# Performance work log

Measured on AMD Instinct MI355X. Metric: run time of the kernel, lower is better.

## Reference

```python
import jax, jax.numpy as jnp
import numpy as np

D_MODEL = 768
D_COND = 128
N_LAYERS = 6
D_STATE = 16
D_CONV = 4
EXPAND = 2
D_INNER = EXPAND * D_MODEL            # 1536
DT_RANK = (D_MODEL + 15) // 16        # 48
BATCH, SEQ = 2, 1024
EPS = 1e-5


def setup_inputs() -> dict:
    key = jax.random.key(0)
    ks = iter(jax.random.split(key, 24))
    rn = lambda shape, s=0.02: jax.random.normal(next(ks), shape, dtype=jnp.float32) * s
    inp = {}
    inp["x"] = jax.random.normal(next(ks), (BATCH, SEQ, D_MODEL), dtype=jnp.float32)
    inp["condition"] = jax.random.normal(next(ks), (BATCH, D_COND), dtype=jnp.float32)
    # per-layer Mamba params, stacked on leading layer dim
    inp["in_proj_w"] = rn((N_LAYERS, 2 * D_INNER, D_MODEL))
    inp["conv_w"] = rn((N_LAYERS, D_INNER, D_CONV), 0.1)
    inp["conv_b"] = jnp.zeros((N_LAYERS, D_INNER), jnp.float32)
    inp["x_proj_w"] = rn((N_LAYERS, DT_RANK + 2 * D_STATE, D_INNER))
    inp["dt_proj_w"] = rn((N_LAYERS, D_INNER, DT_RANK), 0.1)
    inp["dt_proj_b"] = jnp.full((N_LAYERS, D_INNER), -4.0, jnp.float32)  # softplus -> small dt
    inp["A_log"] = jnp.tile(jnp.log(jnp.arange(1, D_STATE + 1, dtype=jnp.float32))[None, None, :], (N_LAYERS, D_INNER, 1))
    inp["D_skip"] = jnp.ones((N_LAYERS, D_INNER), jnp.float32)
    inp["out_proj_w"] = rn((N_LAYERS, D_MODEL, D_INNER))
    # post-residual LayerNorm affine per layer
    inp["norm_w"] = jnp.ones((N_LAYERS, D_MODEL), jnp.float32)
    inp["norm_b"] = jnp.zeros((N_LAYERS, D_MODEL), jnp.float32)
    # AdaLN: condition -> (scale, shift)
    inp["adaln_w"] = rn((N_LAYERS, 2 * D_MODEL, D_COND))
    inp["adaln_b"] = jnp.zeros((N_LAYERS, 2 * D_MODEL), jnp.float32)
    inp["final_norm_w"] = jnp.ones((D_MODEL,), jnp.float32)
    inp["final_norm_b"] = jnp.zeros((D_MODEL,), jnp.float32)
    return inp


def _ln(h, w, b):
    mu = jnp.mean(h, -1, keepdims=True)
    var = jnp.mean(jnp.square(h - mu), -1, keepdims=True)
    return (h - mu) * jax.lax.rsqrt(var + EPS) * w + b


def _ln_noaffine(h):
    mu = jnp.mean(h, -1, keepdims=True)
    var = jnp.mean(jnp.square(h - mu), -1, keepdims=True)
    return (h - mu) * jax.lax.rsqrt(var + EPS)


def _mamba(x, in_w, cw, cb, xp_w, dtp_w, dtp_b, A_log, D_skip, out_w):
    b, l, _ = x.shape
    xz = jnp.einsum('bld,ed->ble', x, in_w)                 # [b,l,2*di]
    xc, z = jnp.split(xz, 2, axis=-1)
    # causal depthwise conv over time
    xc_t = jnp.transpose(xc, (0, 2, 1))                     # [b,di,l]
    xc_t = jax.lax.conv_general_dilated(
        xc_t, cw[:, None, :], window_strides=(1,), padding=[(D_CONV - 1, 0)],
        dimension_numbers=('NCH', 'OIH', 'NCH'), feature_group_count=D_INNER)
    xc = jnp.transpose(xc_t + cb[None, :, None], (0, 2, 1))  # [b,l,di]
    xc = jax.nn.silu(xc)
    dbc = jnp.einsum('bld,ed->ble', xc, xp_w)                # [b,l,dt_rank+2*ds]
    dt = dbc[..., :DT_RANK]
    Bm = dbc[..., DT_RANK:DT_RANK + D_STATE]                 # [b,l,ds]
    Cm = dbc[..., DT_RANK + D_STATE:]                        # [b,l,ds]
    dt = jax.nn.softplus(jnp.einsum('blr,dr->bld', dt, dtp_w) + dtp_b)  # [b,l,di]
    A = -jnp.exp(A_log)                                      # [di,ds]

    def step(h, ts):
        dt_t, B_t, C_t, x_t = ts                             # [b,di],[b,ds],[b,ds],[b,di]
        dA = jnp.exp(dt_t[:, :, None] * A)                   # [b,di,ds]
        h = dA * h + (dt_t * x_t)[:, :, None] * B_t[:, None, :]
        y = jnp.sum(h * C_t[:, None, :], axis=-1)            # [b,di]
        return h, y

    h0 = jnp.zeros((b, D_INNER, D_STATE), x.dtype)
    ts = (jnp.transpose(dt, (1, 0, 2)), jnp.transpose(Bm, (1, 0, 2)),
          jnp.transpose(Cm, (1, 0, 2)), jnp.transpose(xc, (1, 0, 2)))
    h_final, y = jax.lax.scan(step, h0, ts)
    y = jnp.transpose(y, (1, 0, 2)) + D_skip * xc            # [b,l,di]
    y = y * jax.nn.silu(z)
    out = jnp.einsum('bld,ed->ble', y, out_w)                # [b,l,dm]
    return out, h_final


def reference(x, condition, in_proj_w, conv_w, conv_b, x_proj_w, dt_proj_w, dt_proj_b,
              A_log, D_skip, out_proj_w, norm_w, norm_b, adaln_w, adaln_b,
              final_norm_w, final_norm_b):
    h = x
    states = []
    for i in range(N_LAYERS):
        residual = h
        m, st = _mamba(h, in_proj_w[i], conv_w[i], conv_b[i], x_proj_w[i],
                       dt_proj_w[i], dt_proj_b[i], A_log[i], D_skip[i], out_proj_w[i])
        h = _ln(residual + m, norm_w[i], norm_b[i])
        ss = condition @ adaln_w[i].T + adaln_b[i]            # [b,2*dm]
        scale, shift = jnp.split(ss, 2, axis=-1)
        h = _ln_noaffine(h) * (1.0 + scale[:, None, :]) + shift[:, None, :]
        states.append(st)
    h = _ln(h, final_norm_w, final_norm_b)
    return h, jnp.stack(states)
```

## Files before the change

kernel.cpp:

```cpp
#include <hip/hip_runtime.h>
#include <hip/hip_bf16.h>

#define NL 6
#define DM 768
#define DI 1536
#define DS 16
#define NRANK 48
#define DBC 80
#define BATCH 2
#define SEQ 1024
#define NTOK (BATCH*SEQ)
#define NCHUNK 64
#define CHLEN 16
#define XKS 8
#define XKC (DI/XKS)

typedef __attribute__((ext_vector_type(8))) short short8;
typedef __attribute__((ext_vector_type(4))) float f32x4;
typedef __attribute__((ext_vector_type(4))) unsigned short ushort4v;

__device__ inline unsigned short f2bf(float f) {
  union { float f; unsigned u; } x; x.f = f;
  unsigned r = x.u + 0x7FFF + ((x.u >> 16) & 1);
  return (unsigned short)(r >> 16);
}
__device__ inline float bf2f(unsigned short s) {
  union { unsigned u; float f; } x; x.u = ((unsigned)s) << 16;
  return x.f;
}

__device__ inline void gl_lds16(const unsigned short* g, unsigned short* l) {
  __builtin_amdgcn_global_load_lds(
      (const __attribute__((address_space(1))) unsigned int*)(g),
      (__attribute__((address_space(3))) unsigned int*)(l),
      16, 0, 0);
}

#define SPAN_X   (NTOK * DM / 4)
#define SPAN_INW (NL * 2 * DI * DM / 4)
#define SPAN_OUW (NL * DM * DI / 4)
#define SPAN_XPW (NL * DBC * DI / 4)
#define SPAN_ALL (SPAN_X + SPAN_INW + SPAN_OUW + SPAN_XPW)

__device__ inline void cvt4_store(const float* s, unsigned short* d, int i) {
  f32x4 v = ((const f32x4*)s)[i];
  union { ushort4v u4; __hip_bfloat162 h[2]; } u;
  float2 p;
  p.x = v[0]; p.y = v[1]; u.h[0] = __float22bfloat162_rn(p);
  p.x = v[2]; p.y = v[3]; u.h[1] = __float22bfloat162_rn(p);
  ((ushort4v*)d)[i] = u.u4;
}

__global__ __launch_bounds__(256) void cvtall_k(const float* __restrict__ x,
                                                const float* __restrict__ inw,
                                                const float* __restrict__ ouw,
                                                const float* __restrict__ xpw,
                                                unsigned short* __restrict__ xb,
                                                unsigned short* __restrict__ inwb,
                                                unsigned short* __restrict__ ouwb,
                                                unsigned short* __restrict__ xpwb) {
  for (int i = blockIdx.x * 256 + threadIdx.x; i < SPAN_ALL; i += gridDim.x * 256) {
    if (i < SPAN_X) cvt4_store(x, xb, i);
    else if (i < SPAN_X + SPAN_INW) cvt4_store(inw, inwb, i - SPAN_X);
    else if (i < SPAN_X + SPAN_INW + SPAN_OUW) cvt4_store(ouw, ouwb, i - SPAN_X - SPAN_INW);
    else cvt4_store(xpw, xpwb, i - SPAN_X - SPAN_INW - SPAN_OUW);
  }
}

__global__ __launch_bounds__(256) void misc_pre_k(const float* __restrict__ w,
                                                  const float* __restrict__ al,
                                                  unsigned short* __restrict__ wb,
                                                  float* __restrict__ na) {
  int idx = blockIdx.x * 256 + threadIdx.x;
  const int NDT = NL * 1536 * 64;
  if (idx < NDT) {
    int col = idx & 63;
    int row = idx >> 6;
    wb[idx] = (col < NRANK) ? f2bf(w[(size_t)row * NRANK + col]) : (unsigned short)0;
  } else if (idx < NDT + NL * DI * DS) {
    int k = idx - NDT;
    na[k] = -__expf(al[k]);
  }
}

__global__ __launch_bounds__(256) void bt128b_k(
    const unsigned short* __restrict__ A, int lda,
    const unsigned short* __restrict__ W, int ldw,
    unsigned short* __restrict__ C, int ldc,
    int K) {
  __shared__ __align__(16) unsigned short As[2][128 * 32];
  __shared__ __align__(16) unsigned short Ws[2][128 * 32];
  const int tid = threadIdx.x;
  const int bm = blockIdx.y * 128;
  const int bn = blockIdx.x * 128;
  const int lane = tid & 63;
  const int wv = tid >> 6;
  const int wm = (wv >> 1) * 64;
  const int wn = (wv & 1) * 64;
  const int fr = lane & 15;
  const int fs = lane >> 4;

  const int r0 = tid >> 2;
  const int s0 = (tid & 3) ^ (r0 & 3);

  const unsigned short* gA0 = A + (size_t)(bm + r0) * lda + s0 * 8;
  const unsigned short* gA1 = A + (size_t)(bm + r0 + 64) * lda + s0 * 8;
  const unsigned short* gW0 = W + (size_t)(bn + r0) * ldw + s0 * 8;
  const unsigned short* gW1 = W + (size_t)(bn + r0 + 64) * ldw + s0 * 8;

  f32x4 acc[4][4];
#pragma unroll
  for (int i = 0; i < 4; i++)
#pragma unroll
    for (int j = 0; j < 4; j++) acc[i][j] = (f32x4){0.f, 0.f, 0.f, 0.f};

  gl_lds16(gA0, &As[0][0] + tid * 8);
  gl_lds16(gA1, &As[0][2048] + tid * 8);
  gl_lds16(gW0, &Ws[0][0] + tid * 8);
  gl_lds16(gW1, &Ws[0][2048] + tid * 8);
  __syncthreads();

  const int nk = K >> 5;
  int buf = 0;
  for (int kk = 0; kk < nk; kk++) {
    if (kk + 1 < nk) {
      const int k0 = (kk + 1) * 32;
      gl_lds16(gA0 + k0, &As[buf ^ 1][0] + tid * 8);
      gl_lds16(gA1 + k0, &As[buf ^ 1][2048] + tid * 8);
      gl_lds16(gW0 + k0, &Ws[buf ^ 1][0] + tid * 8);
      gl_lds16(gW1 + k0, &Ws[buf ^ 1][2048] + tid * 8);
    }

    short8 af[4], bf[4];
#pragma unroll
    for (int i = 0; i < 4; i++) {
      int rowa = wm + i * 16 + fr;
      af[i] = *(const short8*)&As[buf][rowa * 32 + ((fs ^ (rowa & 3)) * 8)];
      int rowb = wn + i * 16 + fr;
      bf[i] = *(const short8*)&Ws[buf][rowb * 32 + ((fs ^ (rowb & 3)) * 8)];
    }
#pragma unroll
    for (int i = 0; i < 4; i++)
#pragma unroll
      for (int j = 0; j < 4; j++)
        acc[i][j] = __builtin_amdgcn_mfma_f32_16x16x32_bf16(af[i], bf[j], acc[i][j], 0, 0, 0);

    __syncthreads();
    buf ^= 1;
  }

#pragma unroll
  for (int i = 0; i < 4; i++) {
#pragma unroll
    for (int j = 0; j < 4; j++) {
#pragma unroll
      for (int r = 0; r < 4; r++) {
        int row = bm + wm + i * 16 + fs * 4 + r;
        int col = bn + wn + j * 16 + fr;
        C[(size_t)row * ldc + col] = f2bf(acc[i][j][r]);
      }
    }
  }
}

template<int EPI>
__global__ __launch_bounds__(256) void bt64_k(
    const unsigned short* __restrict__ A, int lda,
    const unsigned short* __restrict__ W, int ldw,
    void* __restrict__ Cv, int ldc,
    int K,
    const float* __restrict__ bias,
    const float* __restrict__ resid) {
  __shared__ __align__(16) unsigned short As[2][64 * 32];
  __shared__ __align__(16) unsigned short Ws[2][64 * 32];
  const int tid = threadIdx.x;
  const int bm = blockIdx.y * 64;
  const int bn = blockIdx.x * 64;
  const int lane = tid & 63;
  const int wv = tid >> 6;
  const int wm = (wv >> 1) * 32;
  const int wn = (wv & 1) * 32;
  const int fr = lane & 15;
  const int fs = lane >> 4;

  const int r0 = tid >> 2;
  const int s0 = (tid & 3) ^ (r0 & 3);

  const unsigned short* gA = A + (size_t)(bm + r0) * lda + s0 * 8;
  const unsigned short* gW = W + (size_t)(bn + r0) * ldw + s0 * 8;

  f32x4 acc[2][2];
#pragma unroll
  for (int i = 0; i < 2; i++)
#pragma unroll
    for (int j = 0; j < 2; j++) acc[i][j] = (f32x4){0.f, 0.f, 0.f, 0.f};

  gl_lds16(gA, &As[0][0] + tid * 8);
  gl_lds16(gW, &Ws[0][0] + tid * 8);
  __syncthreads();

  const int nk = K >> 5;
  int buf = 0;
  for (int kk = 0; kk < nk; kk++) {
    if (kk + 1 < nk) {
      const int k0 = (kk + 1) * 32;
      gl_lds16(gA + k0, &As[buf ^ 1][0] + tid * 8);
      gl_lds16(gW + k0, &Ws[buf ^ 1][0] + tid * 8);
    }

    short8 af[2], bf[2];
#pragma unroll
    for (int i = 0; i < 2; i++) {
      int rowa = wm + i * 16 + fr;
      af[i] = *(const short8*)&As[buf][rowa * 32 + ((fs ^ (rowa & 3)) * 8)];
      int rowb = wn + i * 16 + fr;
      bf[i] = *(const short8*)&Ws[buf][rowb * 32 + ((fs ^ (rowb & 3)) * 8)];
    }
#pragma unroll
    for (int i = 0; i < 2; i++)
#pragma unroll
      for (int j = 0; j < 2; j++)
        acc[i][j] = __builtin_amdgcn_mfma_f32_16x16x32_bf16(af[i], bf[j], acc[i][j], 0, 0, 0);

    __syncthreads();
    buf ^= 1;
  }

#pragma unroll
  for (int i = 0; i < 2; i++) {
#pragma unroll
    for (int j = 0; j < 2; j++) {
#pragma unroll
      for (int r = 0; r < 4; r++) {
        int row = bm + wm + i * 16 + fs * 4 + r;
        int col = bn + wn + j * 16 + fr;
        float v = acc[i][j][r];
        if (EPI == 1) {
          float xv = v + bias[col];
          float sp = (xv > 20.f) ? xv : log1pf(__expf(xv));
          ((unsigned short*)Cv)[(size_t)row * ldc + col] = f2bf(sp);
        }
        if (EPI == 2) {
          ((float*)Cv)[(size_t)row * ldc + col] = v + resid[(size_t)row * ldc + col];
        }
      }
    }
  }
}

__global__ __launch_bounds__(256) void xp_k(
    const unsigned short* __restrict__ A,
    const unsigned short* __restrict__ W,
    float* __restrict__ part) {
  __shared__ __align__(16) unsigned short As[64][40];
  __shared__ __align__(16) unsigned short Ws[80][40];
  const int tid = threadIdx.x;
  const int ks = blockIdx.x;
  const int bm = blockIdx.y * 64;
  const int lane = tid & 63;
  const int wv = tid >> 6;
  const int fr = lane & 15;
  const int fs = lane >> 4;
  const int fk = fs * 8;

  const int ar = tid >> 2;
  const int ac = (tid & 3) * 8;
  const int k0base = ks * XKC;

  const unsigned short* gA  = A + (size_t)(bm + ar) * DI + k0base + ac;
  const unsigned short* gW0 = W + (size_t)ar * DI + k0base + ac;
  const unsigned short* gW1 = W + (size_t)(64 + ar) * DI + k0base + ac;

  f32x4 acc[5];
#pragma unroll
  for (int n = 0; n < 5; n++) acc[n] = (f32x4){0.f, 0.f, 0.f, 0.f};

  short8 aA, w0A, w1A;
  aA = *(const short8*)(gA);
  w0A = *(const short8*)(gW0);
  if (tid < 64) w1A = *(const short8*)(gW1);

  const int nk = XKC / 32;
  for (int kk = 0; kk < nk; kk++) {
    __syncthreads();
    *(short8*)&As[ar][ac] = aA;
    *(short8*)&Ws[ar][ac] = w0A;
    if (tid < 64) *(short8*)&Ws[64 + ar][ac] = w1A;
    __syncthreads();

    if (kk + 1 < nk) {
      const int k0 = (kk + 1) * 32;
      aA = *(const short8*)(gA + k0);
      w0A = *(const short8*)(gW0 + k0);
      if (tid < 64) w1A = *(const short8*)(gW1 + k0);
    }

    short8 af = *(const short8*)&As[wv * 16 + fr][fk];
#pragma unroll
    for (int n = 0; n < 5; n++) {
      short8 bf = *(const short8*)&Ws[n * 16 + fr][fk];
      acc[n] = __builtin_amdgcn_mfma_f32_16x16x32_bf16(af, bf, acc[n], 0, 0, 0);
    }
  }

#pragma unroll
  for (int n = 0; n < 5; n++) {
#pragma unroll
    for (int r = 0; r < 4; r++) {
      int row = bm + wv * 16 + fs * 4 + r;
      part[((size_t)ks * NTOK + row) * DBC + n * 16 + fr] = acc[n][r];
    }
  }
}

__global__ __launch_bounds__(256) void xp_reduce_k(const float* __restrict__ part,
                                                   float* __restrict__ dbc,
                                                   unsigned short* __restrict__ dtA) {
  int i = blockIdx.x * 256 + threadIdx.x;
  const f32x4* p4 = (const f32x4*)part;
  const int stride4 = NTOK * DBC / 4;
  f32x4 s = p4[i];
#pragma unroll
  for (int ks = 1; ks < XKS; ks++) {
    f32x4 v = p4[(size_t)ks * stride4 + i];
    s[0] += v[0]; s[1] += v[1]; s[2] += v[2]; s[3] += v[3];
  }
  ((f32x4*)dbc)[i] = s;
  int c4 = (i * 4) % DBC;
  int m = (i * 4) / DBC;
  if (c4 < 64) {
    union { ushort4v u4; __hip_bfloat162 h[2]; } u;
    if (c4 < NRANK) {
      float2 p;
      p.x = s[0]; p.y = s[1]; u.h[0] = __float22bfloat162_rn(p);
      p.x = s[2]; p.y = s[3]; u.h[1] = __float22bfloat162_rn(p);
    } else {
      u.u4 = (ushort4v){0, 0, 0, 0};
    }
    *(ushort4v*)&dtA[(size_t)m * 64 + c4] = u.u4;
  }
}

__global__ __launch_bounds__(256) void conv_silu_k(const unsigned short* __restrict__ xz,
                                                   const float* __restrict__ cw,
                                                   const float* __restrict__ cb,
                                                   unsigned short* __restrict__ xcb) {
  const int d = blockIdx.x * 256 + threadIdx.x;
  const int l0 = blockIdx.y * 16;
  const int b = blockIdx.z;
  const size_t mbase = (size_t)b * SEQ;
  const float w0 = cw[d * 4 + 0], w1 = cw[d * 4 + 1];
  const float w2 = cw[d * 4 + 2], w3 = cw[d * 4 + 3];
  const float bias = cb[d];
  float c3 = (l0 >= 3) ? bf2f(xz[(mbase + l0 - 3) * (2 * DI) + d]) : 0.f;
  float c2 = (l0 >= 2) ? bf2f(xz[(mbase + l0 - 2) * (2 * DI) + d]) : 0.f;
  float c1 = (l0 >= 1) ? bf2f(xz[(mbase + l0 - 1) * (2 * DI) + d]) : 0.f;
#pragma unroll
  for (int t = 0; t < 16; t++) {
    const int l = l0 + t;
    float cur = bf2f(xz[(mbase + l) * (2 * DI) + d]);
    float s = bias + w0 * c3 + w1 * c2 + w2 * c1 + w3 * cur;
    float sig = 1.f / (1.f + __expf(-s));
    xcb[(mbase + l) * DI + d] = f2bf(s * sig);
    c3 = c2; c2 = c1; c1 = cur;
  }
}

__global__ __launch_bounds__(256) void scan1_k(const unsigned short* __restrict__ dt,
                                               const unsigned short* __restrict__ xc,
                                               const float* __restrict__ dbc,
                                               const float* __restrict__ negA_l,
                                               float* __restrict__ cumA,
                                               float* __restrict__ hloc,
                                               unsigned short* __restrict__ yloc,
                                               float* __restrict__ cumdt) {
  __shared__ float Bs[CHLEN][DS];
  __shared__ float Cs[CHLEN][DS];
  const int tid = threadIdx.x;
  const int j = blockIdx.x;
  const int cg = blockIdx.y;
  const int b = cg / 6;
  const int d = (cg % 6) * 256 + tid;
  const int c = b * DI + d;
  const int m0 = b * SEQ + j * CHLEN;

#pragma unroll
  for (int e = tid; e < CHLEN * 32; e += 256) {
    int row = e >> 5, col = e & 31;
    float v = dbc[(size_t)(m0 + row) * DBC + NRANK + col];
    if (col < DS) Bs[row][col] = v; else Cs[row][col - DS] = v;
  }

  float Av[DS];
  const float* na = negA_l + (size_t)d * DS;
#pragma unroll
  for (int s = 0; s < DS; s++) Av[s] = na[s];
  const float Av0 = Av[0];
  bool fast = true;
#pragma unroll
  for (int s = 0; s < DS; s++)
    fast = fast && (fabsf(Av[s] - (s + 1) * Av0) <= 1e-4f * (s + 1));

  float dts[CHLEN], xcs[CHLEN];
#pragma unroll
  for (int t = 0; t < CHLEN; t++) {
    dts[t] = bf2f(dt[(size_t)(m0 + t) * DI + d]);
    xcs[t] = bf2f(xc[(size_t)(m0 + t) * DI + d]);
  }
  __syncthreads();

  float h[DS];
#pragma unroll
  for (int s = 0; s < DS; s++) h[s] = 0.f;
  float cd = 0.f;

  for (int t = 0; t < CHLEN; t++) {
    float dtv = dts[t];
    cd += dtv;
    float dtx = dtv * xcs[t];
    float ysum = 0.f;
    if (fast) {
      float e1 = __expf(dtv * Av0);
      float dA = e1;
      h[0] = fmaf(dA, h[0], dtx * Bs[t][0]);
      ysum = fmaf(h[0], Cs[t][0], ysum);
#pragma unroll
      for (int s = 1; s < DS; s++) {
        dA *= e1;
        h[s] = fmaf(dA, h[s], dtx * Bs[t][s]);
        ysum = fmaf(h[s], Cs[t][s], ysum);
      }
    } else {
#pragma unroll
      for (int s = 0; s < DS; s++) {
        float dA = __expf(dtv * Av[s]);
        h[s] = fmaf(dA, h[s], dtx * Bs[t][s]);
        ysum = fmaf(h[s], Cs[t][s], ysum);
      }
    }
    size_t mi = (size_t)(m0 + t) * DI + d;
    yloc[mi] = f2bf(ysum);
    cumdt[mi] = cd;
  }

  size_t base = ((size_t)j * (BATCH * DI) + c) * DS;
#pragma unroll
  for (int s = 0; s < DS; s++) {
    cumA[base + s] = __expf(cd * Av[s]);
    hloc[base + s] = h[s];
  }
}

__global__ __launch_bounds__(256) void scan2_k(const float* __restrict__ cumA,
                                               const float* __restrict__ hloc,
                                               float* __restrict__ hin,
                                               float* __restrict__ states_out) {
  int idx = blockIdx.x * 256 + threadIdx.x;
  const int stride = BATCH * DI * DS;
  float h = 0.f;
  for (int j = 0; j < NCHUNK; j++) {
    hin[(size_t)j * stride + idx] = h;
    h = fmaf(cumA[(size_t)j * stride + idx], h, hloc[(size_t)j * stride + idx]);
  }
  states_out[idx] = h;
}

__global__ __launch_bounds__(256) void scanfix_k(const unsigned short* __restrict__ yloc,
                                                 const float* __restrict__ cumdt,
                                                 const unsigned short* __restrict__ xc,
                                                 const unsigned short* __restrict__ xz,
                                                 const float* __restrict__ dbc,
                                                 const float* __restrict__ negA_l,
                                                 const float* __restrict__ Dsk,
                                                 const float* __restrict__ hin,
                                                 unsigned short* __restrict__ y) {
  int idx = blockIdx.x * 256 + threadIdx.x;
  int d = idx % DI;
  int m = idx / DI;
  int b = m / SEQ;
  int j = (m % SEQ) / CHLEN;
  float cd = cumdt[idx];
  float yv = bf2f(yloc[idx]);
  const f32x4* na4 = (const f32x4*)(negA_l + (size_t)d * DS);
  const f32x4* cp4 = (const f32x4*)(dbc + (size_t)m * DBC + NRANK + DS);
  const f32x4* h4  = (const f32x4*)(hin + ((size_t)j * (BATCH * DI) + (size_t)b * DI + d) * DS);
  float corr = 0.f;
#pragma unroll
  for (int q = 0; q < 4; q++) {
    f32x4 na = na4[q], cp = cp4[q], hh = h4[q];
#pragma unroll
    for (int e = 0; e < 4; e++)
      corr = fmaf(__expf(cd * na[e]) * hh[e], cp[e], corr);
  }
  yv += corr;
  float xv = bf2f(xc[idx]);
  float zv = bf2f(xz[(size_t)m * (2 * DI) + DI + d]);
  float sig = 1.f / (1.f + __expf(-zv));
  y[idx] = f2bf((yv + Dsk[d] * xv) * (zv * sig));
}

template<bool ADA>
__global__ __launch_bounds__(256) void ln_k(const float* __restrict__ in,
                                            const float* __restrict__ w,
                                            const float* __restrict__ bb,
                                            const float* __restrict__ ss,
                                            float* __restrict__ out,
                                            unsigned short* __restrict__ outb) {
  __shared__ float red[8];
  const int row = blockIdx.x;
  const int bt = row / SEQ;
  const int tid = threadIdx.x;
  const float* x = in + (size_t)row * DM;
  float v[3];
#pragma unroll
  for (int i = 0; i < 3; i++) v[i] = x[tid + i * 256];
  float s1 = v[0] + v[1] + v[2];
  float s2 = v[0]*v[0] + v[1]*v[1] + v[2]*v[2];
#pragma unroll
  for (int o = 32; o > 0; o >>= 1) { s1 += __shfl_down(s1, o); s2 += __shfl_down(s2, o); }
  int wv = tid >> 6, ln = tid & 63;
  if (ln == 0) { red[wv*2] = s1; red[wv*2+1] = s2; }
  __syncthreads();
  s1 = red[0] + red[2] + red[4] + red[6];
  s2 = red[1] + red[3] + red[5] + red[7];
  float mu = s1 * (1.f / DM);
  float var = s2 * (1.f / DM) - mu * mu;
  float rs = rsqrtf(var + 1e-5f);
  float t[3];
#pragma unroll
  for (int i = 0; i < 3; i++) {
    int c = tid + i * 256;
    t[i] = (v[i] - mu) * rs * w[c] + bb[c];
  }
  if (!ADA) {
#pragma unroll
    for (int i = 0; i < 3; i++) out[(size_t)row * DM + tid + i * 256] = t[i];
    return;
  }
  __syncthreads();
  s1 = t[0] + t[1] + t[2];
  s2 = t[0]*t[0] + t[1]*t[1] + t[2]*t[2];
#pragma unroll
  for (int o = 32; o > 0; o >>= 1) { s1 += __shfl_down(s1, o); s2 += __shfl_down(s2, o); }
  if (ln == 0) { red[wv*2] = s1; red[wv*2+1] = s2; }
  __syncthreads();
  s1 = red[0] + red[2] + red[4] + red[6];
  s2 = red[1] + red[3] + red[5] + red[7];
  float mu2 = s1 * (1.f / DM);
  float var2 = s2 * (1.f / DM) - mu2 * mu2;
  float rs2 = rsqrtf(var2 + 1e-5f);
#pragma unroll
  for (int i = 0; i < 3; i++) {
    int c = tid + i * 256;
    float sc = ss[bt * (2 * DM) + c];
    float sh = ss[bt * (2 * DM) + DM + c];
    float r = (t[i] - mu2) * rs2 * (1.f + sc) + sh;
    out[(size_t)row * DM + c] = r;
    outb[(size_t)row * DM + c] = f2bf(r);
  }
}

__global__ __launch_bounds__(256) void adaln_pre_k(const float* __restrict__ cond,
                                                   const float* __restrict__ aw,
                                                   const float* __restrict__ ab,
                                                   float* __restrict__ ss) {
  int idx = blockIdx.x * 256 + threadIdx.x;
  int e = idx % (2 * DM);
  int b = (idx / (2 * DM)) % BATCH;
  int l = idx / (BATCH * 2 * DM);
  const float* c = cond + b * 128;
  const float* wp = aw + ((size_t)l * (2 * DM) + e) * 128;
  float s = ab[l * (2 * DM) + e];
  for (int k = 0; k < 128; k++) s = fmaf(c[k], wp[k], s);
  ss[idx] = s;
}

extern "C" void kernel_launch(void* const* d_in, const int* in_sizes, int n_in,
                              void* d_out, int out_size, void* d_ws, size_t ws_size,
                              hipStream_t stream) {
  const float* x      = (const float*)d_in[0];
  const float* cond   = (const float*)d_in[1];
  const float* in_w   = (const float*)d_in[2];
  const float* conv_w = (const float*)d_in[3];
  const float* conv_b = (const float*)d_in[4];
  const float* xp_w   = (const float*)d_in[5];
  const float* dtp_w  = (const float*)d_in[6];
  const float* dtp_b  = (const float*)d_in[7];
  const float* A_log  = (const float*)d_in[8];
  const float* Dsk    = (const float*)d_in[9];
  const float* out_w  = (const float*)d_in[10];
  const float* norm_w = (const float*)d_in[11];
  const float* norm_b = (const float*)d_in[12];
  const float* ada_w  = (const float*)d_in[13];
  const float* ada_b  = (const float*)d_in[14];
  const float* fn_w   = (const float*)d_in[15];
  const float* fn_b   = (const float*)d_in[16];

  float* out_h = (float*)d_out;
  float* out_states = out_h + (size_t)NTOK * DM;

  float* p = (float*)d_ws;
  float* h_cur = p; p += (size_t)NTOK * DM;
  float* dbc   = p; p += (size_t)NTOK * DBC;
  float* res2  = p; p += (size_t)NTOK * DM;
  float* cumA  = p; p += (size_t)NCHUNK * BATCH * DI * DS;
  float* hloc  = p; p += (size_t)NCHUNK * BATCH * DI * DS;
  float* hin   = p; p += (size_t)NCHUNK * BATCH * DI * DS;
  float* ss    = p; p += (size_t)NL * BATCH * 2 * DM;
  float* xpart = p; p += (size_t)XKS * NTOK * DBC;
  float* cumdt = p; p += (size_t)NTOK * DI;
  float* negA  = p; p += (size_t)NL * DI * DS;
  unsigned short* q = (unsigned short*)p;
  unsigned short* in_w_bf  = q; q += (size_t)NL * 2 * DI * DM;
  unsigned short* out_w_bf = q; q += (size_t)NL * DM * DI;
  unsigned short* xp_w_bf  = q; q += (size_t)NL * DBC * DI;
  unsigned short* dtw_bf   = q; q += (size_t)NL * DI * 64;
  unsigned short* h_bf     = q; q += (size_t)NTOK * DM;
  unsigned short* xz_bf    = q; q += (size_t)NTOK * 2 * DI;
  unsigned short* xc_bf    = q; q += (size_t)NTOK * DI;
  unsigned short* dtb_bf   = q; q += (size_t)NTOK * DI;
  unsigned short* yloc_bf  = q; q += (size_t)NTOK * DI;
  unsigned short* yb_bf    = q; q += (size_t)NTOK * DI;
  unsigned short* dtA_bf   = q; q += (size_t)NTOK * 64;

  hipMemcpyAsync(h_cur, x, (size_t)NTOK * DM * sizeof(float),
                 hipMemcpyDeviceToDevice, stream);
  adaln_pre_k<<<72, 256, 0, stream>>>(cond, ada_w, ada_b, ss);
  cvtall_k<<<2048, 256, 0, stream>>>(x, in_w, out_w, xp_w,
                                     h_bf, in_w_bf, out_w_bf, xp_w_bf);
  misc_pre_k<<<(NL * 1536 * 64 + NL * DI * DS + 255) / 256, 256, 0, stream>>>(
      dtp_w, A_log, dtw_bf, negA);

  for (int l = 0; l < NL; l++) {
    bt128b_k<<<dim3(24, 16), 256, 0, stream>>>(
        h_bf, DM, in_w_bf + (size_t)l * 2 * DI * DM, DM, xz_bf, 2 * DI, DM);
    conv_silu_k<<<dim3(DI / 256, SEQ / 16, BATCH), 256, 0, stream>>>(
        xz_bf, conv_w + (size_t)l * DI * 4, conv_b + (size_t)l * DI, xc_bf);
    xp_k<<<dim3(XKS, NTOK / 64), 256, 0, stream>>>(
        xc_bf, xp_w_bf + (size_t)l * DBC * DI, xpart);
    xp_reduce_k<<<NTOK * DBC / 4 / 256, 256, 0, stream>>>(xpart, dbc, dtA_bf);
    bt64_k<1><<<dim3(DI / 64, NTOK / 64), 256, 0, stream>>>(
        dtA_bf, 64, dtw_bf + (size_t)l * DI * 64, 64, dtb_bf, DI,
        64, dtp_b + (size_t)l * DI, nullptr);
    scan1_k<<<dim3(NCHUNK, 12), 256, 0, stream>>>(
        dtb_bf, xc_bf, dbc, negA + (size_t)l * DI * DS, cumA, hloc,
        yloc_bf, cumdt);
    scan2_k<<<192, 256, 0, stream>>>(
        cumA, hloc, hin, out_states + (size_t)l * BATCH * DI * DS);
    scanfix_k<<<NTOK * DI / 256, 256, 0, stream>>>(
        yloc_bf, cumdt, xc_bf, xz_bf, dbc, negA + (size_t)l * DI * DS,
        Dsk + (size_t)l * DI, hin, yb_bf);
    bt64_k<2><<<dim3(DM / 64, NTOK / 64), 256, 0, stream>>>(
        yb_bf, DI, out_w_bf + (size_t)l * DM * DI, DI, res2, DM,
        DI, nullptr, h_cur);
    ln_k<true><<<NTOK, 256, 0, stream>>>(
        res2, norm_w + (size_t)l * DM, norm_b + (size_t)l * DM,
        ss + (size_t)l * BATCH * 2 * DM, h_cur, h_bf);
  }
  ln_k<false><<<NTOK, 256, 0, stream>>>(h_cur, fn_w, fn_b, nullptr, out_h, nullptr);
}
```

Measured before the change: 865.3 us.

## Fuse three-stage chunked selective scan into one cooperative kernel with grid syncs

Replaces the scan1/scan2/scanfix kernel sequence with a single cooperative kernel that computes per-chunk local scans, syncs the grid, propagates chunk carries, syncs again, then applies corrections and the gating epilogue. The per-chunk y and cumulative dt stay in registers instead of round-tripping through global memory, and two launches per layer go away. In exchange it relies on all 768 blocks being co-resident (launch bounds set to 3 waves/SIMD), and grid-wide syncs add their own latency. It falls back to the old path if the cooperative launch fails.

New measurement: 2.735 ms. 3.16x slower.

```diff
diff --git a/kernel.cpp b/kernel.cpp
--- a/kernel.cpp
+++ b/kernel.cpp
@@ -1,5 +1,6 @@
 #include <hip/hip_runtime.h>
 #include <hip/hip_bf16.h>
+#include <hip/hip_cooperative_groups.h>
 
 #define NL 6
 #define DM 768
@@ -366,6 +367,151 @@
   }
 }
 
+__global__ __launch_bounds__(256, 3) void scanfused_k(
+    const unsigned short* __restrict__ dt,
+    const unsigned short* __restrict__ xc,
+    const float* __restrict__ dbc,
+    const unsigned short* __restrict__ xz,
+    const float* __restrict__ negA_l,
+    const float* __restrict__ Dsk,
+    float* __restrict__ cumA,
+    float* __restrict__ hloc,
+    float* __restrict__ hin,
+    float* __restrict__ states_out,
+    unsigned short* __restrict__ y) {
+  __shared__ float Bs[CHLEN][DS];
+  __shared__ float Cs[CHLEN][DS];
+  const int tid = threadIdx.x;
+  const int j = blockIdx.x;
+  const int cgi = blockIdx.y;
+  const int b = cgi / 6;
+  const int d = (cgi % 6) * 256 + tid;
+  const int c = b * DI + d;
+  const int m0 = b * SEQ + j * CHLEN;
+
+  for (int e = tid; e < CHLEN * 32; e += 256) {
+    int row = e >> 5, col = e & 31;
+    float v = dbc[(size_t)(m0 + row) * DBC + NRANK + col];
+    if (col < DS) Bs[row][col] = v; else Cs[row][col - DS] = v;
+  }
+
+  float Av[DS];
+  const float* na = negA_l + (size_t)d * DS;
+#pragma unroll
+  for (int s = 0; s < DS; s++) Av[s] = na[s];
+  const float Av0 = Av[0];
+  bool fast = true;
+#pragma unroll
+  for (int s = 0; s < DS; s++)
+    fast = fast && (fabsf(Av[s] - (s + 1) * Av0) <= 1e-4f * (s + 1));
+
+  float dts[CHLEN], xcs[CHLEN];
+#pragma unroll
+  for (int t = 0; t < CHLEN; t++) {
+    dts[t] = bf2f(dt[(size_t)(m0 + t) * DI + d]);
+    xcs[t] = bf2f(xc[(size_t)(m0 + t) * DI + d]);
+  }
+  __syncthreads();
+
+  float h[DS];
+#pragma unroll
+  for (int s = 0; s < DS; s++) h[s] = 0.f;
+  float ylocr[CHLEN], cumdtr[CHLEN];
+  float cd = 0.f;
+
+#pragma unroll
+  for (int t = 0; t < CHLEN; t++) {
+    float dtv = dts[t];
+    cd += dtv;
+    float dtx = dtv * xcs[t];
+    float ysum = 0.f;
+    if (fast) {
+      float e1 = __expf(dtv * Av0);
+      float dA = e1;
+      h[0] = fmaf(dA, h[0], dtx * Bs[t][0]);
+      ysum = fmaf(h[0], Cs[t][0], ysum);
+#pragma unroll
+      for (int s = 1; s < DS; s++) {
+        dA *= e1;
+        h[s] = fmaf(dA, h[s], dtx * Bs[t][s]);
+        ysum = fmaf(h[s], Cs[t][s], ysum);
+      }
+    } else {
+#pragma unroll
+      for (int s = 0; s < DS; s++) {
+        float dA = __expf(dtv * Av[s]);
+        h[s] = fmaf(dA, h[s], dtx * Bs[t][s]);
+        ysum = fmaf(h[s], Cs[t][s], ysum);
+      }
+    }
+    ylocr[t] = ysum;
+    cumdtr[t] = cd;
+  }
+
+  size_t base = ((size_t)j * (BATCH * DI) + c) * DS;
+#pragma unroll
+  for (int s = 0; s < DS; s++) {
+    cumA[base + s] = __expf(cd * Av[s]);
+    hloc[base + s] = h[s];
+  }
+
+  __threadfence();
+  cooperative_groups::this_grid().sync();
+
+  int lb = blockIdx.y * gridDim.x + blockIdx.x;
+  if (lb < 192) {
+    int idx = lb * 256 + tid;
+    const int stride = BATCH * DI * DS;
+    float hh = 0.f;
+    for (int jj = 0; jj < NCHUNK; jj++) {
+      hin[(size_t)jj * stride + idx] = hh;
+      hh = fmaf(cumA[(size_t)jj * stride + idx], hh, hloc[(size_t)jj * stride + idx]);
+    }
+    states_out[idx] = hh;
+  }
+
+  __threadfence();
+  cooperative_groups::this_grid().sync();
+
+  const f32x4* h4 = (const f32x4*)(hin + base);
+  f32x4 hv[4];
+#pragma unroll
+  for (int q = 0; q < 4; q++) hv[q] = h4[q];
+  float dval = Dsk[d];
+
+#pragma unroll
+  for (int t = 0; t < CHLEN; t++) {
+    float cdv = cumdtr[t];
+    float corr = 0.f;
+    if (fast) {
+      float e1 = __expf(cdv * Av0);
+      float P = e1;
+#pragma unroll
+      for (int q = 0; q < 4; q++) {
+#pragma unroll
+        for (int e = 0; e < 4; e++) {
+          int s = q * 4 + e;
+          if (s > 0) P *= e1;
+          corr = fmaf(P * hv[q][e], Cs[t][s], corr);
+        }
+      }
+    } else {
+#pragma unroll
+      for (int q = 0; q < 4; q++) {
+#pragma unroll
+        for (int e = 0; e < 4; e++) {
+          int s = q * 4 + e;
+          corr = fmaf(__expf(cdv * Av[s]) * hv[q][e], Cs[t][s], corr);
+        }
+      }
+    }
+    float yv = ylocr[t] + corr;
+    float zv = bf2f(xz[(size_t)(m0 + t) * (2 * DI) + DI + d]);
+    float sig = 1.f / (1.f + __expf(-zv));
+    y[(size_t)(m0 + t) * DI + d] = f2bf((yv + dval * xcs[t]) * (zv * sig));
+  }
+}
+
 __global__ __launch_bounds__(256) void scan1_k(const unsigned short* __restrict__ dt,
                                                const unsigned short* __restrict__ xc,
                                                const float* __restrict__ dbc,
@@ -384,7 +530,6 @@
   const int c = b * DI + d;
   const int m0 = b * SEQ + j * CHLEN;
 
-#pragma unroll
   for (int e = tid; e < CHLEN * 32; e += 256) {
     int row = e >> 5, col = e & 31;
     float v = dbc[(size_t)(m0 + row) * DBC + NRANK + col];
@@ -608,8 +753,8 @@
   float* hin   = p; p += (size_t)NCHUNK * BATCH * DI * DS;
   float* ss    = p; p += (size_t)NL * BATCH * 2 * DM;
   float* xpart = p; p += (size_t)XKS * NTOK * DBC;
+  float* negA  = p; p += (size_t)NL * DI * DS;
   float* cumdt = p; p += (size_t)NTOK * DI;
-  float* negA  = p; p += (size_t)NL * DI * DS;
   unsigned short* q = (unsigned short*)p;
   unsigned short* in_w_bf  = q; q += (size_t)NL * 2 * DI * DM;
   unsigned short* out_w_bf = q; q += (size_t)NL * DM * DI;
@@ -619,8 +764,8 @@
   unsigned short* xz_bf    = q; q += (size_t)NTOK * 2 * DI;
   unsigned short* xc_bf    = q; q += (size_t)NTOK * DI;
   unsigned short* dtb_bf   = q; q += (size_t)NTOK * DI;
+  unsigned short* yb_bf    = q; q += (size_t)NTOK * DI;
   unsigned short* yloc_bf  = q; q += (size_t)NTOK * DI;
-  unsigned short* yb_bf    = q; q += (size_t)NTOK * DI;
   unsigned short* dtA_bf   = q; q += (size_t)NTOK * 64;
 
   hipMemcpyAsync(h_cur, x, (size_t)NTOK * DM * sizeof(float),
@@ -642,14 +787,33 @@
     bt64_k<1><<<dim3(DI / 64, NTOK / 64), 256, 0, stream>>>(
         dtA_bf, 64, dtw_bf + (size_t)l * DI * 64, 64, dtb_bf, DI,
         64, dtp_b + (size_t)l * DI, nullptr);
-    scan1_k<<<dim3(NCHUNK, 12), 256, 0, stream>>>(
-        dtb_bf, xc_bf, dbc, negA + (size_t)l * DI * DS, cumA, hloc,
-        yloc_bf, cumdt);
-    scan2_k<<<192, 256, 0, stream>>>(
-        cumA, hloc, hin, out_states + (size_t)l * BATCH * DI * DS);
-    scanfix_k<<<NTOK * DI / 256, 256, 0, stream>>>(
-        yloc_bf, cumdt, xc_bf, xz_bf, dbc, negA + (size_t)l * DI * DS,
-        Dsk + (size_t)l * DI, hin, yb_bf);
+    {
+      const unsigned short* a0 = dtb_bf;
+      const unsigned short* a1 = xc_bf;
+      const float* a2 = dbc;
+      const unsigned short* a3 = xz_bf;
+      const float* a4 = negA + (size_t)l * DI * DS;
+      const float* a5 = Dsk + (size_t)l * DI;
+      float* a6 = cumA;
+      float* a7 = hloc;
+      float* a8 = hin;
+      float* a9 = out_states + (size_t)l * BATCH * DI * DS;
+      unsigned short* a10 = yb_bf;
+      void* args[] = {&a0, &a1, &a2, &a3, &a4, &a5, &a6, &a7, &a8, &a9, &a10};
+      hipError_t ce = hipLaunchCooperativeKernel((void*)scanfused_k,
+                                                 dim3(NCHUNK, 12), dim3(256),
+                                                 args, 0, stream);
+      if (ce != hipSuccess) {
+        scan1_k<<<dim3(NCHUNK, 12), 256, 0, stream>>>(
+            dtb_bf, xc_bf, dbc, negA + (size_t)l * DI * DS, cumA, hloc,
+            yloc_bf, cumdt);
+        scan2_k<<<192, 256, 0, stream>>>(
+            cumA, hloc, hin, out_states + (size_t)l * BATCH * DI * DS);
+        scanfix_k<<<NTOK * DI / 256, 256, 0, stream>>>(
+            yloc_bf, cumdt, xc_bf, xz_bf, dbc, negA + (size_t)l * DI * DS,
+            Dsk + (size_t)l * DI, hin, yb_bf);
+      }
+    }
     bt64_k<2><<<dim3(DM / 64, NTOK / 64), 256, 0, stream>>>(
         yb_bf, DI, out_w_bf + (size_t)l * DM * DI, DI, res2, DM,
         DI, nullptr, h_cur);
```
